# Performance work log

Hardware: AMD Instinct MI355X
Metric: run time of the kernel (lower is better)

Reference implementation:

```python
import jax, jax.numpy as jnp
import numpy as np

NP = 100000   # total patch-graph nodes
NG = 2000     # number of patch graphs == mesh nodes
EP = 800000   # patch edges
NM = 2000     # mesh nodes
EM = 32000    # mesh edges
FIN = 5       # patch_feat_dim
EPS = 1e-5


def _leaky(x, s):
    return jnp.where(x >= 0, x, s * x)


def _gat(x, W, al, ar, src, dst, n):
    # DGL GATConv (no bias/residual, eval mode): per-head projection,
    # additive attention with LeakyReLU(0.2), segment softmax over incoming
    # edges per destination, weighted scatter-sum.
    H, D = al.shape
    h = (x @ W).reshape(n, H, D)                  # [N,H,D]
    el = (h * al).sum(-1)                         # [N,H]
    er = (h * ar).sum(-1)                         # [N,H]
    e = _leaky(el[src] + er[dst], 0.2)            # [E,H]
    m = jax.ops.segment_max(e, dst, num_segments=n)
    ee = jnp.exp(e - m[dst])
    s = jax.ops.segment_sum(ee, dst, num_segments=n)
    a = ee / jnp.maximum(s, 1e-9)[dst]            # [E,H]
    return jax.ops.segment_sum(h[src] * a[:, :, None], dst, num_segments=n)


def _gnorm(x, g, b, al):
    # GraphNorm over all nodes in the batch (called without graph in source)
    mu = x.mean(0, keepdims=True)
    xc = x - al * mu
    v = (xc * xc).mean(0, keepdims=True)
    return g * xc / jnp.sqrt(v + EPS) + b


def setup_inputs() -> dict:
    key = jax.random.key(0)
    ks = jax.random.split(key, 40)
    w = lambda k, sh: jax.random.normal(k, sh, jnp.float32) * 0.1
    d = {}
    d['node_feats'] = jax.random.normal(ks[0], (NP, FIN), jnp.float32)
    d['patch_src'] = jax.random.randint(ks[1], (EP,), 0, NP)
    d['patch_dst'] = jax.random.randint(ks[2], (EP,), 0, NP)
    d['patch_gid'] = jnp.repeat(jnp.arange(NG), NP // NG)  # 50 nodes/graph
    d['mesh_src'] = jax.random.randint(ks[3], (EM,), 0, NM)
    d['mesh_dst'] = jax.random.randint(ks[4], (EM,), 0, NM)
    # PatchReader2GATLayer (hidden=64): GAT1 4h x64, GAT2 3h x64, GATcls 2h x32
    d['pW1'] = w(ks[5], (FIN, 256)); d['pal1'] = w(ks[6], (4, 64)); d['par1'] = w(ks[7], (4, 64))
    d['pg1_g'] = jnp.ones((256,)); d['pg1_b'] = jnp.zeros((256,)); d['pg1_a'] = jnp.ones((256,))
    d['pW2'] = w(ks[8], (256, 192)); d['pal2'] = w(ks[9], (3, 64)); d['par2'] = w(ks[10], (3, 64))
    d['pg2_g'] = jnp.ones((192,)); d['pg2_b'] = jnp.zeros((192,)); d['pg2_a'] = jnp.ones((192,))
    d['pW3'] = w(ks[11], (192, 64)); d['pal3'] = w(ks[12], (2, 32)); d['par3'] = w(ks[13], (2, 32))
    d['pcls'] = w(ks[14], (32, 32))
    # GraphNormPatchReader (readout_dim=32)
    d['rn_g'] = jnp.ones((32,)); d['rn_b'] = jnp.zeros((32,)); d['rn_a'] = jnp.ones((32,))
    # GraphMeshReader2GATLayer (hidden=64): GAT1 4h x64, GAT2 3h x32, GATcls 2h x32
    d['mW1'] = w(ks[15], (32, 256)); d['mal1'] = w(ks[16], (4, 64)); d['mar1'] = w(ks[17], (4, 64))
    d['mg1_g'] = jnp.ones((256,)); d['mg1_b'] = jnp.zeros((256,)); d['mg1_a'] = jnp.ones((256,))
    d['mW2'] = w(ks[18], (256, 96)); d['mal2'] = w(ks[19], (3, 32)); d['mar2'] = w(ks[20], (3, 32))
    d['mg2_g'] = jnp.ones((96,)); d['mg2_b'] = jnp.zeros((96,)); d['mg2_a'] = jnp.ones((96,))
    d['mW3'] = w(ks[21], (96, 64)); d['mal3'] = w(ks[22], (2, 32)); d['mar3'] = w(ks[23], (2, 32))
    d['mcls'] = w(ks[24], (32, 15))
    return d


def reference(node_feats, patch_src, patch_dst, patch_gid, mesh_src, mesh_dst,
              pW1, pal1, par1, pg1_g, pg1_b, pg1_a,
              pW2, pal2, par2, pg2_g, pg2_b, pg2_a,
              pW3, pal3, par3, pcls, rn_g, rn_b, rn_a,
              mW1, mal1, mar1, mg1_g, mg1_b, mg1_a,
              mW2, mal2, mar2, mg2_g, mg2_b, mg2_a,
              mW3, mal3, mar3, mcls):
    # ---- PatchReader2GATLayer over all batched patch graphs ----
    h = _gat(node_feats, pW1, pal1, par1, patch_src, patch_dst, NP).reshape(NP, -1)
    h = _gnorm(_leaky(h, 0.01), pg1_g, pg1_b, pg1_a)
    h = _gat(h, pW2, pal2, par2, patch_src, patch_dst, NP).reshape(NP, -1)
    h = _gnorm(_leaky(h, 0.01), pg2_g, pg2_b, pg2_a)
    h = _gat(h, pW3, pal3, par3, patch_src, patch_dst, NP).mean(1)  # [NP,32]
    cnt = jax.ops.segment_sum(jnp.ones((NP,), h.dtype), patch_gid, num_segments=NG)
    ro = jax.ops.segment_sum(h, patch_gid, num_segments=NG) / jnp.maximum(cnt, 1.0)[:, None]
    ro = ro @ pcls                                 # [NG,32] per-patch readouts
    ro = _gnorm(_leaky(ro, 0.01), rn_g, rn_b, rn_a)
    # ---- GraphMeshReader2GATLayer over mesh graph ----
    m = _gat(ro, mW1, mal1, mar1, mesh_src, mesh_dst, NM).reshape(NM, -1)
    m = _gnorm(_leaky(m, 0.01), mg1_g, mg1_b, mg1_a)
    m = _gat(m, mW2, mal2, mar2, mesh_src, mesh_dst, NM).reshape(NM, -1)
    m = _gnorm(_leaky(m, 0.01), mg2_g, mg2_b, mg2_a)
    m = _gat(m, mW3, mal3, mar3, mesh_src, mesh_dst, NM).mean(1)    # [NM,32]
    mesh_out = m.mean(0, keepdims=True) @ mcls     # dgl.mean_nodes -> [1,15]
    return (mesh_out, ro)
```

## Files before the change

### kernel.cpp

```cpp
#include <hip/hip_runtime.h>

typedef unsigned short ushort;
typedef unsigned int uint;
typedef __attribute__((ext_vector_type(8))) short short8;
typedef __attribute__((ext_vector_type(4))) float float4v;

#define DEV __device__ __forceinline__

DEV float b2f(ushort u) {
    union { uint i; float f; } v; v.i = ((uint)u) << 16; return v.f;
}
DEV ushort f2b(float f) {
    union { float f; uint i; } v; v.f = f;
    uint x = v.i;
    uint r = x + 0x7fffu + ((x >> 16) & 1u);
    return (ushort)(r >> 16);
}
DEV float leaky(float x, float s) { return x >= 0.f ? x : s * x; }

DEV void gload16(const void* g, void* l) {
    __builtin_amdgcn_global_load_lds((const __attribute__((address_space(1))) void*)g,
                                     (__attribute__((address_space(3))) void*)l, 16, 0, 0);
}

struct ConvArgs {
    const void* s[37];
    float* d[37];
    int n[37];
};

__global__ __launch_bounds__(256) void convert_kernel(ConvArgs a, const ushort* __restrict__ x0,
                                                      int* __restrict__ flag) {
    __shared__ int sfp32;
    int tid = threadIdx.x;
    if (tid < 64) {
        int cnt = 0;
        for (int j = 0; j < 8; j++) {
            ushort u = x0[(tid * 8 + j) * 2];
            int e = (u >> 7) & 0xFF;
            if (e >= 100 && e <= 140) cnt++;
        }
#pragma unroll
        for (int m = 1; m < 64; m <<= 1) cnt += __shfl_xor(cnt, m, 64);
        if (tid == 0) sfp32 = (cnt < 256) ? 1 : 0;
    }
    __syncthreads();
    bool fp32 = (sfp32 != 0);
    if (blockIdx.x == 0 && blockIdx.y == 0 && tid == 0) *flag = fp32 ? 1 : 0;

    int ai = blockIdx.y;
    int n = a.n[ai];
    const void* s = a.s[ai];
    float* d = a.d[ai];
    int stride = gridDim.x * blockDim.x;
    if (s == nullptr) {
        for (int i = blockIdx.x * blockDim.x + tid; i < n; i += stride) d[i] = 0.f;
    } else {
        for (int i = blockIdx.x * blockDim.x + tid; i < n; i += stride)
            d[i] = fp32 ? ((const float*)s)[i] : b2f(((const ushort*)s)[i]);
    }
}

struct PackArgs { const float* W; ushort* O; int K; int N; };
struct Pack5 { PackArgs m[5]; };

__global__ __launch_bounds__(256) void pack5_kernel(Pack5 pa) {
    int mi = blockIdx.y;
    const float* __restrict__ W = pa.m[mi].W;
    ushort* __restrict__ O = pa.m[mi].O;
    int K = pa.m[mi].K, N = pa.m[mi].N;
    int G = (K >> 3) * N;
    for (int gi = blockIdx.x * 256 + threadIdx.x; gi < G; gi += gridDim.x * 256) {
        int kb = gi / N;
        int n = gi - kb * N;
        const float* wp = W + (size_t)(kb * 8) * N + n;
        uint4 pk;
        pk.x = (uint)f2b(wp[0]) | ((uint)f2b(wp[N]) << 16);
        pk.y = (uint)f2b(wp[2 * N]) | ((uint)f2b(wp[3 * N]) << 16);
        pk.z = (uint)f2b(wp[4 * N]) | ((uint)f2b(wp[5 * N]) << 16);
        pk.w = (uint)f2b(wp[6 * N]) | ((uint)f2b(wp[7 * N]) << 16);
        *(uint4*)(O + (size_t)gi * 8) = pk;
    }
}

__global__ __launch_bounds__(256) void hist_both(const int* __restrict__ dstP, int* __restrict__ cntP, int EPc,
                                                 const int* __restrict__ dstM, int* __restrict__ cntM, int EMc,
                                                 int PB) {
    bool patch = (int)blockIdx.x < PB;
    const int* dst = patch ? dstP : dstM;
    int* cnt = patch ? cntP : cntM;
    int E = patch ? EPc : EMc;
    int nb = patch ? PB : gridDim.x - PB;
    int b = patch ? blockIdx.x : blockIdx.x - PB;
    int stride = nb * blockDim.x;
    for (int i = b * blockDim.x + threadIdx.x; i < E; i += stride)
        atomicAdd(&cnt[dst[i]], 1);
}

__global__ __launch_bounds__(256) void scan_both(const int* __restrict__ cntP, int* __restrict__ offP,
                                                 int* __restrict__ bsumP, int nP, int SBP,
                                                 const int* __restrict__ cntM, int* __restrict__ offM,
                                                 int* __restrict__ bsumM, int nM) {
    __shared__ int ls[256];
    bool patch = (int)blockIdx.x < SBP;
    const int* cnt = patch ? cntP : cntM;
    int* off = patch ? offP : offM;
    int* bsum = patch ? bsumP : bsumM;
    int n = patch ? nP : nM;
    int b = patch ? blockIdx.x : blockIdx.x - SBP;
    int t = threadIdx.x;
    int base = b * 2048 + t * 8;
    int v[8];
    int s = 0;
#pragma unroll
    for (int i = 0; i < 8; i++) {
        int idx = base + i;
        v[i] = idx < n ? cnt[idx] : 0;
        s += v[i];
    }
    ls[t] = s;
    __syncthreads();
#pragma unroll
    for (int d = 1; d < 256; d <<= 1) {
        int add = (t >= d) ? ls[t - d] : 0;
        __syncthreads();
        ls[t] += add;
        __syncthreads();
    }
    int run = ls[t] - s;
#pragma unroll
    for (int i = 0; i < 8; i++) {
        int idx = base + i;
        if (idx < n) off[idx] = run;
        run += v[i];
    }
    if (t == 255) bsum[b] = ls[255];
}

__global__ __launch_bounds__(256) void fixup_both(const int* __restrict__ bsumP, int* __restrict__ offP,
                                                  int nP, int SBP,
                                                  const int* __restrict__ bsumM, int* __restrict__ offM,
                                                  int nM, int SBM) {
    bool patch = (int)blockIdx.x < SBP;
    const int* bsum = patch ? bsumP : bsumM;
    int* off = patch ? offP : offM;
    int n = patch ? nP : nM;
    int nb = patch ? SBP : SBM;
    int b = patch ? blockIdx.x : blockIdx.x - SBP;
    int t = threadIdx.x;
    int base = 0;
    for (int i = 0; i < b; i++) base += bsum[i];
    int idx0 = b * 2048 + t * 8;
    if (base != 0) {
#pragma unroll
        for (int i = 0; i < 8; i++) {
            int idx = idx0 + i;
            if (idx < n) off[idx] += base;
        }
    }
    if (b == nb - 1 && t == 255) off[n] = base + bsum[b];
}

__global__ __launch_bounds__(256) void scatter_both(const int* __restrict__ srcP, const int* __restrict__ dstP,
                                                    const int* __restrict__ offP, int* __restrict__ curP,
                                                    int* __restrict__ csrP, int EPc,
                                                    const int* __restrict__ srcM, const int* __restrict__ dstM,
                                                    const int* __restrict__ offM, int* __restrict__ curM,
                                                    int* __restrict__ csrM, int EMc, int PB) {
    bool patch = (int)blockIdx.x < PB;
    const int* src = patch ? srcP : srcM;
    const int* dst = patch ? dstP : dstM;
    const int* off = patch ? offP : offM;
    int* cursor = patch ? curP : curM;
    int* csr = patch ? csrP : csrM;
    int E = patch ? EPc : EMc;
    int nb = patch ? PB : gridDim.x - PB;
    int b = patch ? blockIdx.x : blockIdx.x - PB;
    int stride = nb * blockDim.x;
    for (int i = b * blockDim.x + threadIdx.x; i < E; i += stride) {
        int d = dst[i];
        int pos = off[d] + atomicAdd(&cursor[d], 1);
        csr[pos] = src[i];
    }
}

__global__ __launch_bounds__(256) void proj1_elr_kernel(const float* __restrict__ x,
                                                        const float* __restrict__ W,
                                                        const float* __restrict__ al,
                                                        const float* __restrict__ ar,
                                                        float* __restrict__ el,
                                                        float* __restrict__ er, int Nn) {
    int t = threadIdx.x;
    int head = t >> 6, lane = t & 63;
    float wv[5];
#pragma unroll
    for (int k = 0; k < 5; k++) wv[k] = W[k * 256 + t];
    float alv = al[t];
    float arv = ar[t];
    int n0 = blockIdx.x * 4;
    int n1 = min(n0 + 4, Nn);
    for (int n = n0; n < n1; n++) {
        float acc = 0.f;
#pragma unroll
        for (int k = 0; k < 5; k++) acc += x[n * 5 + k] * wv[k];
        float pl = acc * alv, pr = acc * arv;
#pragma unroll
        for (int m = 1; m < 64; m <<= 1) {
            pl += __shfl_xor(pl, m, 64);
            pr += __shfl_xor(pr, m, 64);
        }
        if (lane == 0) { el[n * 4 + head] = pl; er[n * 4 + head] = pr; }
    }
}

__global__ __launch_bounds__(256, 4) void aggr1_fly_kernel(const float* __restrict__ x,
                                                           const float* __restrict__ W,
                                                           const float* __restrict__ el,
                                                           const float* __restrict__ er,
                                                           const int* __restrict__ off,
                                                           const int* __restrict__ csr,
                                                           float* __restrict__ out, int Nn) {
    int wid = threadIdx.x >> 6;
    int lane = threadIdx.x & 63;
    int grp = lane / 20;
    int gl = lane - grp * 20;
    int dbase = blockIdx.x * 12 + wid * 3;
    int d = dbase + grp;
    bool accl = (grp < 3) && (d < Nn);
    int dd = accl ? d : 0;
    int h_ = gl / 5, k_ = gl - h_ * 5;
    int c0 = lane * 4;
    int myhead = lane >> 4;
    float w0[5], w1[5], w2[5], w3[5];
#pragma unroll
    for (int k = 0; k < 5; k++) {
        float4 wv = *(const float4*)(W + k * 256 + c0);
        w0[k] = wv.x; w1[k] = wv.y; w2[k] = wv.z; w3[k] = wv.w;
    }
    float erd = accl ? er[dd * 4 + h_] : 0.f;
    float acc = 0.f, sh = 0.f;
    int e = accl ? off[dd] : 0;
    int e1 = accl ? off[dd + 1] : 0;
#define A1_ACC(XV, EV)                                  \
    {                                                   \
        float e0_ = (EV) + erd;                         \
        e0_ = e0_ >= 0.f ? e0_ : 0.2f * e0_;            \
        float w_ = __expf(fminf(e0_, 80.f));            \
        acc += w_ * (XV);                               \
        sh += w_;                                       \
    }
    for (; e + 4 <= e1; e += 4) {
        int s0 = csr[e], s1 = csr[e + 1], s2 = csr[e + 2], s3 = csr[e + 3];
        float x0 = x[s0 * 5 + k_];
        float x1 = x[s1 * 5 + k_];
        float x2 = x[s2 * 5 + k_];
        float x3 = x[s3 * 5 + k_];
        float v0 = el[s0 * 4 + h_];
        float v1 = el[s1 * 4 + h_];
        float v2 = el[s2 * 4 + h_];
        float v3 = el[s3 * 4 + h_];
        A1_ACC(x0, v0) A1_ACC(x1, v1) A1_ACC(x2, v2) A1_ACC(x3, v3)
    }
    for (; e < e1; e++) {
        int s0 = csr[e];
        float x0 = x[s0 * 5 + k_];
        float v0 = el[s0 * 4 + h_];
        A1_ACC(x0, v0)
    }
#undef A1_ACC
#pragma unroll
    for (int g3 = 0; g3 < 3; g3++) {
        int dsto = dbase + g3;
        if (dsto >= Nn) break;
        float a_k[5];
#pragma unroll
        for (int k = 0; k < 5; k++) a_k[k] = __shfl(acc, g3 * 20 + myhead * 5 + k, 64);
        float s = __shfl(sh, g3 * 20 + myhead * 5, 64);
        float inv = 1.f / fmaxf(s, 1e-9f);
        float o0 = 0.f, o1 = 0.f, o2 = 0.f, o3 = 0.f;
#pragma unroll
        for (int k = 0; k < 5; k++) {
            o0 += a_k[k] * w0[k]; o1 += a_k[k] * w1[k];
            o2 += a_k[k] * w2[k]; o3 += a_k[k] * w3[k];
        }
        float4 o;
        o.x = leaky(o0 * inv, 0.01f);
        o.y = leaky(o1 * inv, 0.01f);
        o.z = leaky(o2 * inv, 0.01f);
        o.w = leaky(o3 * inv, 0.01f);
        *(float4*)(out + (size_t)dsto * 256 + c0) = o;
    }
}

template <int H, int LOGD, int HD>
__global__ __launch_bounds__(256, 4) void aggr4_kernel(const ushort* __restrict__ h,
                                                       const float* __restrict__ el,
                                                       const float* __restrict__ er,
                                                       const int* __restrict__ off,
                                                       const int* __restrict__ csr,
                                                       float* __restrict__ out, int Nn,
                                                       float oslope) {
    int wid = threadIdx.x >> 6;
    int lane = threadIdx.x & 63;
    int half = lane >> 5, hl = lane & 31;
    constexpr int NL = HD / 8;
    int d = blockIdx.x * 8 + wid * 2 + half;
    bool valid = (hl < NL) && (d < Nn);
    int dd = valid ? d : 0;
    int myhead = (hl * 8) >> LOGD;
    float erd = valid ? er[dd * H + myhead] : 0.f;
    float a0 = 0.f, a1 = 0.f, a2 = 0.f, a3 = 0.f;
    float a4 = 0.f, a5 = 0.f, a6 = 0.f, a7 = 0.f, s = 0.f;
    int e = valid ? off[dd] : 0;
    int e1 = valid ? off[dd + 1] : 0;
#define A8_ACC(EV, HR)                                      \
    {                                                       \
        float ev_ = (EV) + erd;                             \
        ev_ = ev_ >= 0.f ? ev_ : 0.2f * ev_;                \
        float w_ = __expf(fminf(ev_, 80.f));                \
        a0 += w_ * b2f((ushort)(HR).x);                     \
        a1 += w_ * b2f((ushort)((HR).x >> 16));             \
        a2 += w_ * b2f((ushort)(HR).y);                     \
        a3 += w_ * b2f((ushort)((HR).y >> 16));             \
        a4 += w_ * b2f((ushort)(HR).z);                     \
        a5 += w_ * b2f((ushort)((HR).z >> 16));             \
        a6 += w_ * b2f((ushort)(HR).w);                     \
        a7 += w_ * b2f((ushort)((HR).w >> 16));             \
        s += w_;                                            \
    }
#define A8_ACCM(OK, EV, HR)                                 \
    {                                                       \
        float ev_ = (EV) + erd;                             \
        ev_ = ev_ >= 0.f ? ev_ : 0.2f * ev_;                \
        float w_ = (OK) ? __expf(fminf(ev_, 80.f)) : 0.f;   \
        a0 += w_ * b2f((ushort)(HR).x);                     \
        a1 += w_ * b2f((ushort)((HR).x >> 16));             \
        a2 += w_ * b2f((ushort)(HR).y);                     \
        a3 += w_ * b2f((ushort)((HR).y >> 16));             \
        a4 += w_ * b2f((ushort)(HR).z);                     \
        a5 += w_ * b2f((ushort)((HR).z >> 16));             \
        a6 += w_ * b2f((ushort)(HR).w);                     \
        a7 += w_ * b2f((ushort)((HR).w >> 16));             \
        s += w_;                                            \
    }
    for (; e + 4 <= e1; e += 4) {
        int s0 = csr[e], s1 = csr[e + 1], s2 = csr[e + 2], s3 = csr[e + 3];
        float e0 = el[s0 * H + myhead];
        float e1v = el[s1 * H + myhead];
        float e2v = el[s2 * H + myhead];
        float e3v = el[s3 * H + myhead];
        uint4 h0 = *(const uint4*)(h + (size_t)s0 * HD + hl * 8);
        uint4 h1 = *(const uint4*)(h + (size_t)s1 * HD + hl * 8);
        uint4 h2 = *(const uint4*)(h + (size_t)s2 * HD + hl * 8);
        uint4 h3 = *(const uint4*)(h + (size_t)s3 * HD + hl * 8);
        A8_ACC(e0, h0) A8_ACC(e1v, h1) A8_ACC(e2v, h2) A8_ACC(e3v, h3)
    }
    if (e < e1) {
        bool k1 = e + 1 < e1, k2 = e + 2 < e1, k3 = e + 3 < e1;
        int s0 = csr[e];
        int s1 = csr[k1 ? e + 1 : e];
        int s2 = csr[k2 ? e + 2 : e];
        int s3 = csr[k3 ? e + 3 : e];
        float e0 = el[s0 * H + myhead];
        float e1v = el[s1 * H + myhead];
        float e2v = el[s2 * H + myhead];
        float e3v = el[s3 * H + myhead];
        uint4 h0 = *(const uint4*)(h + (size_t)s0 * HD + hl * 8);
        uint4 h1 = *(const uint4*)(h + (size_t)s1 * HD + hl * 8);
        uint4 h2 = *(const uint4*)(h + (size_t)s2 * HD + hl * 8);
        uint4 h3 = *(const uint4*)(h + (size_t)s3 * HD + hl * 8);
        A8_ACCM(true, e0, h0) A8_ACCM(k1, e1v, h1) A8_ACCM(k2, e2v, h2) A8_ACCM(k3, e3v, h3)
    }
#undef A8_ACC
#undef A8_ACCM
    if (valid) {
        float inv = 1.f / fmaxf(s, 1e-9f);
        float4 oa, ob;
        oa.x = leaky(a0 * inv, oslope);
        oa.y = leaky(a1 * inv, oslope);
        oa.z = leaky(a2 * inv, oslope);
        oa.w = leaky(a3 * inv, oslope);
        ob.x = leaky(a4 * inv, oslope);
        ob.y = leaky(a5 * inv, oslope);
        ob.z = leaky(a6 * inv, oslope);
        ob.w = leaky(a7 * inv, oslope);
        float* po = out + (size_t)dd * HD + hl * 8;
        *(float4*)(po) = oa;
        *(float4*)(po + 4) = ob;
    }
}

__global__ __launch_bounds__(256, 4) void aggr_mean_kernel(const ushort* __restrict__ h,
                                                           const float* __restrict__ el,
                                                           const float* __restrict__ er,
                                                           const int* __restrict__ off,
                                                           const int* __restrict__ csr,
                                                           const int* __restrict__ gid,
                                                           float* __restrict__ out_sum,
                                                           float* __restrict__ out_cnt,
                                                           int Nn) {
    __shared__ float red[8][32];
    __shared__ int gids[8];
    int wid = threadIdx.x >> 6;
    int lane = threadIdx.x & 63;
    int half = lane >> 5;
    int hl = lane & 31;
    int row = wid * 2 + half;
    int d = blockIdx.x * 8 + row;
    bool valid = d < Nn;
    int dd = valid ? d : 0;
    int head = hl >> 4;
    float erd = er[dd * 2 + head];
    float a0 = 0.f, a1 = 0.f, s = 0.f;
    int e = valid ? off[dd] : 0;
    int e1 = valid ? off[dd + 1] : 0;
#define AM_ACC(Q, V)                                        \
    {                                                       \
        float ev_ = (head ? (Q).y : (Q).x) + erd;           \
        ev_ = ev_ >= 0.f ? ev_ : 0.2f * ev_;                \
        float w_ = __expf(fminf(ev_, 80.f));                \
        a0 += w_ * b2f((ushort)(V));                        \
        a1 += w_ * b2f((ushort)((V) >> 16));                \
        s += w_;                                            \
    }
#define AM_ACCM(OK, Q, V)                                   \
    {                                                       \
        float ev_ = (head ? (Q).y : (Q).x) + erd;           \
        ev_ = ev_ >= 0.f ? ev_ : 0.2f * ev_;                \
        float w_ = (OK) ? __expf(fminf(ev_, 80.f)) : 0.f;   \
        a0 += w_ * b2f((ushort)(V));                        \
        a1 += w_ * b2f((ushort)((V) >> 16));                \
        s += w_;                                            \
    }
    for (; e + 8 <= e1; e += 8) {
        int s0 = csr[e], s1 = csr[e + 1], s2 = csr[e + 2], s3 = csr[e + 3];
        int s4 = csr[e + 4], s5 = csr[e + 5], s6 = csr[e + 6], s7 = csr[e + 7];
        float2 q0 = *(const float2*)(el + s0 * 2);
        float2 q1 = *(const float2*)(el + s1 * 2);
        float2 q2 = *(const float2*)(el + s2 * 2);
        float2 q3 = *(const float2*)(el + s3 * 2);
        float2 q4 = *(const float2*)(el + s4 * 2);
        float2 q5 = *(const float2*)(el + s5 * 2);
        float2 q6 = *(const float2*)(el + s6 * 2);
        float2 q7 = *(const float2*)(el + s7 * 2);
        uint v0 = *(const uint*)(h + (size_t)s0 * 64 + hl * 2);
        uint v1 = *(const uint*)(h + (size_t)s1 * 64 + hl * 2);
        uint v2 = *(const uint*)(h + (size_t)s2 * 64 + hl * 2);
        uint v3 = *(const uint*)(h + (size_t)s3 * 64 + hl * 2);
        uint v4 = *(const uint*)(h + (size_t)s4 * 64 + hl * 2);
        uint v5 = *(const uint*)(h + (size_t)s5 * 64 + hl * 2);
        uint v6 = *(const uint*)(h + (size_t)s6 * 64 + hl * 2);
        uint v7 = *(const uint*)(h + (size_t)s7 * 64 + hl * 2);
        AM_ACC(q0, v0) AM_ACC(q1, v1) AM_ACC(q2, v2) AM_ACC(q3, v3)
        AM_ACC(q4, v4) AM_ACC(q5, v5) AM_ACC(q6, v6) AM_ACC(q7, v7)
    }
    if (e < e1) {
        bool k1 = e + 1 < e1, k2 = e + 2 < e1, k3 = e + 3 < e1;
        bool k4 = e + 4 < e1, k5 = e + 5 < e1, k6 = e + 6 < e1, k7 = e + 7 < e1;
        int s0 = csr[e];
        int s1 = csr[k1 ? e + 1 : e];
        int s2 = csr[k2 ? e + 2 : e];
        int s3 = csr[k3 ? e + 3 : e];
        int s4 = csr[k4 ? e + 4 : e];
        int s5 = csr[k5 ? e + 5 : e];
        int s6 = csr[k6 ? e + 6 : e];
        int s7 = csr[k7 ? e + 7 : e];
        float2 q0 = *(const float2*)(el + s0 * 2);
        float2 q1 = *(const float2*)(el + s1 * 2);
        float2 q2 = *(const float2*)(el + s2 * 2);
        float2 q3 = *(const float2*)(el + s3 * 2);
        float2 q4 = *(const float2*)(el + s4 * 2);
        float2 q5 = *(const float2*)(el + s5 * 2);
        float2 q6 = *(const float2*)(el + s6 * 2);
        float2 q7 = *(const float2*)(el + s7 * 2);
        uint v0 = *(const uint*)(h + (size_t)s0 * 64 + hl * 2);
        uint v1 = *(const uint*)(h + (size_t)s1 * 64 + hl * 2);
        uint v2 = *(const uint*)(h + (size_t)s2 * 64 + hl * 2);
        uint v3 = *(const uint*)(h + (size_t)s3 * 64 + hl * 2);
        uint v4 = *(const uint*)(h + (size_t)s4 * 64 + hl * 2);
        uint v5 = *(const uint*)(h + (size_t)s5 * 64 + hl * 2);
        uint v6 = *(const uint*)(h + (size_t)s6 * 64 + hl * 2);
        uint v7 = *(const uint*)(h + (size_t)s7 * 64 + hl * 2);
        AM_ACCM(true, q0, v0) AM_ACCM(k1, q1, v1) AM_ACCM(k2, q2, v2) AM_ACCM(k3, q3, v3)
        AM_ACCM(k4, q4, v4) AM_ACCM(k5, q5, v5) AM_ACCM(k6, q6, v6) AM_ACCM(k7, q7, v7)
    }
#undef AM_ACC
#undef AM_ACCM
    float inv = 1.f / fmaxf(s, 1e-9f);
    float y0 = a0 * inv, y1 = a1 * inv;
    float p0 = __shfl(y0, lane + 16, 64);
    float p1 = __shfl(y1, lane + 16, 64);
    if (hl < 16) {
        red[row][2 * hl] = valid ? 0.5f * (y0 + p0) : 0.f;
        red[row][2 * hl + 1] = valid ? 0.5f * (y1 + p1) : 0.f;
        if (hl == 0) gids[row] = valid ? (gid ? gid[d] : 0) : -1;
    }
    __syncthreads();
    if (threadIdx.x < 32) {
        int c = threadIdx.x;
        float sum = 0.f;
        int cur = gids[0];
#pragma unroll
        for (int r = 0; r < 8; r++) {
            int gr = gids[r];
            if (gr != cur) {
                if (cur >= 0) atomicAdd(&out_sum[cur * 32 + c], sum);
                sum = 0.f;
                cur = gr;
            }
            if (gr >= 0) sum += red[r][c];
        }
        if (cur >= 0) atomicAdd(&out_sum[cur * 32 + c], sum);
    } else if (threadIdx.x == 32 && out_cnt) {
        float cnt = 0.f;
        int cur = gids[0];
#pragma unroll
        for (int r = 0; r < 8; r++) {
            int gr = gids[r];
            if (gr != cur) {
                if (cur >= 0) atomicAdd(&out_cnt[cur], cnt);
                cnt = 0.f;
                cur = gr;
            }
            if (gr >= 0) cnt += 1.f;
        }
        if (cur >= 0) atomicAdd(&out_cnt[cur], cnt);
    }
}

__global__ void colstats_kernel(const float* __restrict__ x,
                                float* __restrict__ sum,
                                float* __restrict__ sumsq, int Nn) {
    int C = blockDim.x, c = threadIdx.x;
    int nb = gridDim.x;
    int chunk = (Nn + nb - 1) / nb;
    int r0 = blockIdx.x * chunk;
    int r1 = min(r0 + chunk, Nn);
    float ls = 0.f, lq = 0.f;
    int r = r0;
    for (; r + 8 <= r1; r += 8) {
        const float* p = x + (size_t)r * C + c;
        float v0 = p[0];
        float v1 = p[C];
        float v2 = p[2 * C];
        float v3 = p[3 * C];
        float v4 = p[4 * C];
        float v5 = p[5 * C];
        float v6 = p[6 * C];
        float v7 = p[7 * C];
        ls += ((v0 + v1) + (v2 + v3)) + ((v4 + v5) + (v6 + v7));
        lq += ((v0 * v0 + v1 * v1) + (v2 * v2 + v3 * v3)) +
              ((v4 * v4 + v5 * v5) + (v6 * v6 + v7 * v7));
    }
    for (; r < r1; r++) {
        float v = x[(size_t)r * C + c];
        ls += v; lq += v * v;
    }
    atomicAdd(&sum[c], ls);
    atomicAdd(&sumsq[c], lq);
}

__global__ void gnorm_apply_ro_kernel(const float* __restrict__ x,
                                      const float* __restrict__ sum,
                                      const float* __restrict__ sumsq,
                                      const float* __restrict__ g,
                                      const float* __restrict__ b,
                                      const float* __restrict__ a,
                                      void* __restrict__ doutv,
                                      const int* __restrict__ flag,
                                      float* __restrict__ rof, int Nn) {
    int c = threadIdx.x;
    float invn = 1.f / (float)Nn;
    float mu = sum[c] * invn, ex2 = sumsq[c] * invn;
    float av = a[c];
    float var = ex2 - 2.f * av * mu * mu + av * av * mu * mu;
    float sc = g[c] * rsqrtf(var + 1e-5f);
    float sh = b[c] - sc * av * mu;
    bool fp32 = (*flag != 0);
    for (int r = blockIdx.x; r < Nn; r += gridDim.x) {
        int i = r * 32 + c;
        float v = x[i] * sc + sh;
        rof[i] = v;
        if (fp32) ((float*)doutv)[15 + i] = v;
        else      ((ushort*)doutv)[15 + i] = f2b(v);
    }
}

__global__ __launch_bounds__(256) void readout_kernel(const float* __restrict__ ro_sum,
                                                      const float* __restrict__ ro_cnt,
                                                      const float* __restrict__ pcls,
                                                      float* __restrict__ ro_lin, int NGc) {
    int idx = blockIdx.x * blockDim.x + threadIdx.x;
    int g = idx >> 5, c = idx & 31;
    if (g >= NGc) return;
    float inv = 1.f / fmaxf(ro_cnt[g], 1.f);
    float acc = 0.f;
#pragma unroll
    for (int k = 0; k < 32; k++) acc += ro_sum[g * 32 + k] * inv * pcls[k * 32 + c];
    ro_lin[g * 32 + c] = leaky(acc, 0.01f);
}

template <int K, int N, int H, int LOGD, bool GN>
__global__ __launch_bounds__(256, 4) void gemm_bf_kernel(const float* __restrict__ A,
                                                         const ushort* __restrict__ Bc,
                                                         const float* __restrict__ csum,
                                                         const float* __restrict__ g,
                                                         const float* __restrict__ gb,
                                                         const float* __restrict__ ga,
                                                         const float* __restrict__ al,
                                                         const float* __restrict__ ar,
                                                         ushort* __restrict__ C,
                                                         float* __restrict__ el,
                                                         float* __restrict__ er, int M) {
    constexpr int NT = N / 16;
    constexpr int T = K / 32;
    constexpr int BG = 4 * N;
    constexpr int RB = (BG + 255) / 256;
    __shared__ __align__(16) ushort Blds[2][BG * 8];
    __shared__ float ScL[K], ShL[K];
    int tid = threadIdx.x;
    int w = tid >> 6, lane = tid & 63, q = lane >> 4, l16 = lane & 15;
    int m0 = blockIdx.x * 64;
    if constexpr (GN) {
        if (tid < K) {
            float invn = 1.f / (float)M;
            float mu = csum[tid] * invn, ex2 = csum[512 + tid] * invn;
            float av = ga[tid];
            float var = ex2 - 2.f * av * mu * mu + av * av * mu * mu;
            float sc = g[tid] * rsqrtf(var + 1e-5f);
            ScL[tid] = sc;
            ShL[tid] = gb[tid] - sc * av * mu;
        }
    }
    int row = m0 + w * 16 + l16;
    const float* ap = A + (size_t)(row < M ? row : 0) * K + q * 8;

#pragma unroll
    for (int rb = 0; rb < RB; rb++) {
        int gidx = rb * 256 + tid;
        if (BG % 256 == 0 || gidx < BG) gload16(Bc + (size_t)gidx * 8, &Blds[0][gidx * 8]);
    }
    float4 a0 = *(const float4*)(ap);
    float4 a1 = *(const float4*)(ap + 4);
    float4v acc[NT];
#pragma unroll
    for (int nt = 0; nt < NT; nt++) acc[nt] = (float4v){0.f, 0.f, 0.f, 0.f};
    __syncthreads();

    int cur = 0;
    for (int t = 0; t < T; t++) {
        float4 n0, n1;
        bool more = (t + 1 < T);
        if (more) {
#pragma unroll
            for (int rb = 0; rb < RB; rb++) {
                int gidx = rb * 256 + tid;
                if (BG % 256 == 0 || gidx < BG)
                    gload16(Bc + (size_t)((t + 1) * BG + gidx) * 8, &Blds[cur ^ 1][gidx * 8]);
            }
            n0 = *(const float4*)(ap + (t + 1) * 32);
            n1 = *(const float4*)(ap + (t + 1) * 32 + 4);
        }
        if constexpr (GN) {
            int kc = t * 32 + q * 8;
            float4 sc0 = *(const float4*)(&ScL[kc]);
            float4 sc1 = *(const float4*)(&ScL[kc + 4]);
            float4 sh0 = *(const float4*)(&ShL[kc]);
            float4 sh1 = *(const float4*)(&ShL[kc + 4]);
            a0.x = a0.x * sc0.x + sh0.x;
            a0.y = a0.y * sc0.y + sh0.y;
            a0.z = a0.z * sc0.z + sh0.z;
            a0.w = a0.w * sc0.w + sh0.w;
            a1.x = a1.x * sc1.x + sh1.x;
            a1.y = a1.y * sc1.y + sh1.y;
            a1.z = a1.z * sc1.z + sh1.z;
            a1.w = a1.w * sc1.w + sh1.w;
        }
        union { uint4 u; short8 s; } cvt;
        cvt.u.x = (uint)f2b(a0.x) | ((uint)f2b(a0.y) << 16);
        cvt.u.y = (uint)f2b(a0.z) | ((uint)f2b(a0.w) << 16);
        cvt.u.z = (uint)f2b(a1.x) | ((uint)f2b(a1.y) << 16);
        cvt.u.w = (uint)f2b(a1.z) | ((uint)f2b(a1.w) << 16);
        short8 av = cvt.s;
#pragma unroll
        for (int nt = 0; nt < NT; nt++) {
            short8 bv = *(const short8*)(&Blds[cur][(q * N + nt * 16 + l16) * 8]);
            acc[nt] = __builtin_amdgcn_mfma_f32_16x16x32_bf16(av, bv, acc[nt], 0, 0, 0);
        }
        __syncthreads();
        if (more) { a0 = n0; a1 = n1; }
        cur ^= 1;
    }
    float pel[4][H], per[4][H];
#pragma unroll
    for (int i = 0; i < 4; i++)
#pragma unroll
        for (int hh = 0; hh < H; hh++) { pel[i][hh] = 0.f; per[i][hh] = 0.f; }
#pragma unroll
    for (int nt = 0; nt < NT; nt++) {
        int col = nt * 16 + l16;
        float alc = al[col], arc = ar[col];
        constexpr int HSH = LOGD - 4;
        int hh = nt >> HSH;
#pragma unroll
        for (int i = 0; i < 4; i++) {
            int orow = m0 + w * 16 + q * 4 + i;
            float v = acc[nt][i];
            if (orow < M) C[(size_t)orow * N + col] = f2b(v);
            pel[i][hh] += v * alc;
            per[i][hh] += v * arc;
        }
    }
#pragma unroll
    for (int i = 0; i < 4; i++) {
#pragma unroll
        for (int hh = 0; hh < H; hh++) {
            float vl = pel[i][hh], vr = per[i][hh];
#pragma unroll
            for (int m = 1; m < 16; m <<= 1) {
                vl += __shfl_xor(vl, m, 64);
                vr += __shfl_xor(vr, m, 64);
            }
            if (l16 == 0) {
                int orow = m0 + w * 16 + q * 4 + i;
                if (orow < M) { el[orow * H + hh] = vl; er[orow * H + hh] = vr; }
            }
        }
    }
}

__global__ __launch_bounds__(64) void final_kernel(const float* __restrict__ msum,
                                                   const float* __restrict__ mcls,
                                                   void* __restrict__ doutv,
                                                   const int* __restrict__ flag, int Nm) {
    int t = threadIdx.x;
    if (t < 15) {
        float inv = 1.f / (float)Nm;
        float acc = 0.f;
#pragma unroll
        for (int c = 0; c < 32; c++) acc += msum[c] * inv * mcls[c * 15 + t];
        if (*flag) ((float*)doutv)[t] = acc;
        else       ((ushort*)doutv)[t] = f2b(acc);
    }
}

extern "C" void kernel_launch(void* const* d_in, const int* in_sizes, int n_in,
                              void* d_out, int out_size, void* d_ws, size_t ws_size,
                              hipStream_t stream) {
    const int NP = 100000, NG = 2000, EP = 800000, NM = 2000, EM = 32000;

    const int* patch_src = (const int*)d_in[1];
    const int* patch_dst = (const int*)d_in[2];
    const int* patch_gid = (const int*)d_in[3];
    const int* mesh_src = (const int*)d_in[4];
    const int* mesh_dst = (const int*)d_in[5];

    char* p = (char*)d_ws;
    auto alloc = [&](size_t bytes) -> char* {
        char* r = p;
        p += (bytes + 255) & ~(size_t)255;
        return r;
    };
    char* zbase = p;
    int* cnt_p = (int*)alloc((size_t)NP * 4);
    int* cursor_p = (int*)alloc((size_t)NP * 4);
    int* cnt_m = (int*)alloc((size_t)NM * 4);
    int* cursor_m = (int*)alloc((size_t)NM * 4);
    float* ro_sum = (float*)alloc((size_t)NG * 32 * 4);
    float* ro_cnt = (float*)alloc((size_t)NG * 4);
    float* msum = (float*)alloc(32 * 4);
    float* colbuf = (float*)alloc(6 * 1024 * 4);
    size_t zbytes = (size_t)(p - zbase);
    int* flag = (int*)alloc(256);
    int* off_p = (int*)alloc((size_t)(NP + 1) * 4);
    int* off_m = (int*)alloc((size_t)(NM + 1) * 4);
    int* bsum_p = (int*)alloc(64 * 4);
    int* bsum_m = (int*)alloc(16 * 4);
    int* csr_p = (int*)alloc((size_t)EP * 4);
    int* csr_m = (int*)alloc((size_t)EM * 4);
    float* el = (float*)alloc((size_t)NP * 4 * 4);
    float* er = (float*)alloc((size_t)NP * 4 * 4);
    ushort* hbuf = (ushort*)alloc((size_t)NP * 256 * 2);
    float* gbuf = (float*)alloc((size_t)NP * 256 * 4);
    ushort* hm = (ushort*)alloc((size_t)NM * 256 * 2);
    float* gm = (float*)alloc((size_t)NM * 256 * 4);
    float* elm = (float*)alloc((size_t)NM * 4 * 4);
    float* erm = (float*)alloc((size_t)NM * 4 * 4);
    float* ro_lin = (float*)alloc((size_t)NG * 32 * 4);
    float* ro_f = (float*)alloc((size_t)NG * 32 * 4);
    ushort* Bp2 = (ushort*)alloc(256 * 192 * 2);
    ushort* Bp3 = (ushort*)alloc(192 * 64 * 2);
    ushort* Bm1 = (ushort*)alloc(32 * 256 * 2);
    ushort* Bm2 = (ushort*)alloc(256 * 96 * 2);
    ushort* Bm3 = (ushort*)alloc(96 * 64 * 2);

    ConvArgs ca;
    float* convp[36];
    int conv_idx[36];
    conv_idx[0] = 0;
    for (int i = 1; i < 36; i++) conv_idx[i] = 5 + i;
    for (int j = 0; j < 36; j++) {
        int ii = conv_idx[j];
        int n = in_sizes[ii];
        float* dd = (float*)alloc((size_t)n * 4);
        ca.s[j] = d_in[ii];
        ca.d[j] = dd;
        ca.n[j] = n;
        convp[j] = dd;
    }
    ca.s[36] = nullptr;
    ca.d[36] = (float*)zbase;
    ca.n[36] = (int)(zbytes / 4);

    const float* xf = convp[0];
    const float *pW1f = convp[1], *pal1f = convp[2], *par1f = convp[3];
    const float *pg1_gf = convp[4], *pg1_bf = convp[5], *pg1_af = convp[6];
    const float *pW2f = convp[7], *pal2f = convp[8], *par2f = convp[9];
    const float *pg2_gf = convp[10], *pg2_bf = convp[11], *pg2_af = convp[12];
    const float *pW3f = convp[13], *pal3f = convp[14], *par3f = convp[15];
    const float* pclsf = convp[16];
    const float *rn_gf = convp[17], *rn_bf2 = convp[18], *rn_af = convp[19];
    const float *mW1f = convp[20], *mal1f = convp[21], *mar1f = convp[22];
    const float *mg1_gf = convp[23], *mg1_bf = convp[24], *mg1_af = convp[25];
    const float *mW2f = convp[26], *mal2f = convp[27], *mar2f = convp[28];
    const float *mg2_gf = convp[29], *mg2_bf = convp[30], *mg2_af = convp[31];
    const float *mW3f = convp[32], *mal3f = convp[33], *mar3f = convp[34];
    const float* mclsf = convp[35];

    convert_kernel<<<dim3(16, 37), 256, 0, stream>>>(ca, (const ushort*)d_in[0], flag);

    Pack5 p5;
    p5.m[0] = {pW2f, Bp2, 256, 192};
    p5.m[1] = {pW3f, Bp3, 192, 64};
    p5.m[2] = {mW1f, Bm1, 32, 256};
    p5.m[3] = {mW2f, Bm2, 256, 96};
    p5.m[4] = {mW3f, Bm3, 96, 64};
    pack5_kernel<<<dim3(48, 5), 256, 0, stream>>>(p5);

    const int SBP = (NP + 2047) / 2048, SBM = (NM + 2047) / 2048;
    hist_both<<<512 + 64, 256, 0, stream>>>(patch_dst, cnt_p, EP, mesh_dst, cnt_m, EM, 512);
    scan_both<<<SBP + SBM, 256, 0, stream>>>(cnt_p, off_p, bsum_p, NP, SBP, cnt_m, off_m, bsum_m, NM);
    fixup_both<<<SBP + SBM, 256, 0, stream>>>(bsum_p, off_p, NP, SBP, bsum_m, off_m, NM, SBM);
    scatter_both<<<512 + 64, 256, 0, stream>>>(patch_src, patch_dst, off_p, cursor_p, csr_p, EP,
                                               mesh_src, mesh_dst, off_m, cursor_m, csr_m, EM, 512);

    int gP = (NP + 3) / 4;
    int gP12 = (NP + 11) / 12;
    int gA2 = (NP + 7) / 8, gA2m = (NM + 7) / 8;
    int gP2 = (NP + 7) / 8, gM2 = (NM + 7) / 8;
    int gT = (NP + 63) / 64, gTm = (NM + 63) / 64;
    float* cb0 = colbuf + 0 * 1024;
    float* cb1 = colbuf + 1 * 1024;
    float* cb2 = colbuf + 2 * 1024;
    float* cb3 = colbuf + 3 * 1024;
    float* cb4 = colbuf + 4 * 1024;

    proj1_elr_kernel<<<gP, 256, 0, stream>>>(xf, pW1f, pal1f, par1f, el, er, NP);
    aggr1_fly_kernel<<<gP12, 256, 0, stream>>>(xf, pW1f, el, er, off_p, csr_p, gbuf, NP);
    colstats_kernel<<<512, 256, 0, stream>>>(gbuf, cb0, cb0 + 512, NP);

    gemm_bf_kernel<256, 192, 3, 6, true><<<gT, 256, 0, stream>>>(
        gbuf, Bp2, cb0, pg1_gf, pg1_bf, pg1_af, pal2f, par2f, hbuf, el, er, NP);
    aggr4_kernel<3, 6, 192><<<gA2, 256, 0, stream>>>(hbuf, el, er, off_p, csr_p, gbuf, NP, 0.01f);
    colstats_kernel<<<512, 192, 0, stream>>>(gbuf, cb1, cb1 + 512, NP);

    gemm_bf_kernel<192, 64, 2, 5, true><<<gT, 256, 0, stream>>>(
        gbuf, Bp3, cb1, pg2_gf, pg2_bf, pg2_af, pal3f, par3f, hbuf, el, er, NP);
    aggr_mean_kernel<<<gP2, 256, 0, stream>>>(hbuf, el, er, off_p, csr_p, patch_gid,
                                              ro_sum, ro_cnt, NP);

    readout_kernel<<<(NG * 32 + 255) / 256, 256, 0, stream>>>(ro_sum, ro_cnt, pclsf, ro_lin, NG);
    colstats_kernel<<<64, 32, 0, stream>>>(ro_lin, cb2, cb2 + 512, NG);
    gnorm_apply_ro_kernel<<<64, 32, 0, stream>>>(ro_lin, cb2, cb2 + 512, rn_gf, rn_bf2, rn_af,
                                                 d_out, flag, ro_f, NG);

    gemm_bf_kernel<32, 256, 4, 6, false><<<gTm, 256, 0, stream>>>(
        ro_f, Bm1, nullptr, nullptr, nullptr, nullptr, mal1f, mar1f, hm, elm, erm, NM);
    aggr4_kernel<4, 6, 256><<<gA2m, 256, 0, stream>>>(hm, elm, erm, off_m, csr_m, gm, NM, 0.01f);
    colstats_kernel<<<64, 256, 0, stream>>>(gm, cb3, cb3 + 512, NM);

    gemm_bf_kernel<256, 96, 3, 5, true><<<gTm, 256, 0, stream>>>(
        gm, Bm2, cb3, mg1_gf, mg1_bf, mg1_af, mal2f, mar2f, hm, elm, erm, NM);
    aggr4_kernel<3, 5, 96><<<gA2m, 256, 0, stream>>>(hm, elm, erm, off_m, csr_m, gm, NM, 0.01f);
    colstats_kernel<<<64, 96, 0, stream>>>(gm, cb4, cb4 + 512, NM);

    gemm_bf_kernel<96, 64, 2, 5, true><<<gTm, 256, 0, stream>>>(
        gm, Bm3, cb4, mg2_gf, mg2_bf, mg2_af, mal3f, mar3f, hm, elm, erm, NM);
    aggr_mean_kernel<<<gM2, 256, 0, stream>>>(hm, elm, erm, off_m, csr_m, nullptr,
                                              msum, nullptr, NM);
    final_kernel<<<1, 64, 0, stream>>>(msum, mclsf, d_out, flag, NM);

    (void)n_in; (void)out_size; (void)ws_size;
}
```

Baseline: 645.3 us.

## Fuse GraphNorm column statistics into aggregation kernels and precompute W·a for layer-1 attention

```diff
diff --git a/kernel.cpp b/kernel.cpp
--- a/kernel.cpp
+++ b/kernel.cpp
@@ -80,6 +80,25 @@
         pk.z = (uint)f2b(wp[4 * N]) | ((uint)f2b(wp[5 * N]) << 16);
         pk.w = (uint)f2b(wp[6 * N]) | ((uint)f2b(wp[7 * N]) << 16);
         *(uint4*)(O + (size_t)gi * 8) = pk;
+    }
+}
+
+__global__ __launch_bounds__(64) void prep_elr_kernel(const float* __restrict__ W,
+                                                      const float* __restrict__ al,
+                                                      const float* __restrict__ ar,
+                                                      float* __restrict__ wal,
+                                                      float* __restrict__ war) {
+    int t = threadIdx.x;
+    if (t < 20) {
+        int k = t >> 2, h = t & 3;
+        float sl = 0.f, sr = 0.f;
+        for (int d = 0; d < 64; d++) {
+            float w = W[k * 256 + h * 64 + d];
+            sl += w * al[h * 64 + d];
+            sr += w * ar[h * 64 + d];
+        }
+        wal[t] = sl;
+        war[t] = sr;
     }
 }
 
@@ -184,33 +203,32 @@
     }
 }
 
-__global__ __launch_bounds__(256) void proj1_elr_kernel(const float* __restrict__ x,
-                                                        const float* __restrict__ W,
-                                                        const float* __restrict__ al,
-                                                        const float* __restrict__ ar,
-                                                        float* __restrict__ el,
-                                                        float* __restrict__ er, int Nn) {
-    int t = threadIdx.x;
-    int head = t >> 6, lane = t & 63;
-    float wv[5];
-#pragma unroll
-    for (int k = 0; k < 5; k++) wv[k] = W[k * 256 + t];
-    float alv = al[t];
-    float arv = ar[t];
-    int n0 = blockIdx.x * 4;
-    int n1 = min(n0 + 4, Nn);
-    for (int n = n0; n < n1; n++) {
-        float acc = 0.f;
-#pragma unroll
-        for (int k = 0; k < 5; k++) acc += x[n * 5 + k] * wv[k];
-        float pl = acc * alv, pr = acc * arv;
-#pragma unroll
-        for (int m = 1; m < 64; m <<= 1) {
-            pl += __shfl_xor(pl, m, 64);
-            pr += __shfl_xor(pr, m, 64);
-        }
-        if (lane == 0) { el[n * 4 + head] = pl; er[n * 4 + head] = pr; }
-    }
+__global__ __launch_bounds__(256) void proj1b_kernel(const float* __restrict__ x,
+                                                     const float* __restrict__ wal,
+                                                     const float* __restrict__ war,
+                                                     float* __restrict__ el,
+                                                     float* __restrict__ er, int Nn) {
+    int n = blockIdx.x * 256 + threadIdx.x;
+    if (n >= Nn) return;
+    float xv[5];
+#pragma unroll
+    for (int k = 0; k < 5; k++) xv[k] = x[n * 5 + k];
+    float l0 = 0.f, l1 = 0.f, l2 = 0.f, l3 = 0.f;
+    float r0 = 0.f, r1 = 0.f, r2 = 0.f, r3 = 0.f;
+#pragma unroll
+    for (int k = 0; k < 5; k++) {
+        float xk = xv[k];
+        l0 += xk * wal[k * 4 + 0];
+        l1 += xk * wal[k * 4 + 1];
+        l2 += xk * wal[k * 4 + 2];
+        l3 += xk * wal[k * 4 + 3];
+        r0 += xk * war[k * 4 + 0];
+        r1 += xk * war[k * 4 + 1];
+        r2 += xk * war[k * 4 + 2];
+        r3 += xk * war[k * 4 + 3];
+    }
+    *(float4*)(el + n * 4) = make_float4(l0, l1, l2, l3);
+    *(float4*)(er + n * 4) = make_float4(r0, r1, r2, r3);
 }
 
 __global__ __launch_bounds__(256, 4) void aggr1_fly_kernel(const float* __restrict__ x,
@@ -219,7 +237,10 @@
                                                            const float* __restrict__ er,
                                                            const int* __restrict__ off,
                                                            const int* __restrict__ csr,
-                                                           float* __restrict__ out, int Nn) {
+                                                           float* __restrict__ out,
+                                                           float* __restrict__ cstat, int Nn) {
+    __shared__ float s1m[4][256];
+    __shared__ float s1q[4][256];
     int wid = threadIdx.x >> 6;
     int lane = threadIdx.x & 63;
     int grp = lane / 20;
@@ -268,6 +289,8 @@
         A1_ACC(x0, v0)
     }
 #undef A1_ACC
+    float ls0 = 0.f, ls1 = 0.f, ls2 = 0.f, ls3 = 0.f;
+    float lq0 = 0.f, lq1 = 0.f, lq2 = 0.f, lq3 = 0.f;
 #pragma unroll
     for (int g3 = 0; g3 < 3; g3++) {
         int dsto = dbase + g3;
@@ -289,7 +312,21 @@
         o.z = leaky(o2 * inv, 0.01f);
         o.w = leaky(o3 * inv, 0.01f);
         *(float4*)(out + (size_t)dsto * 256 + c0) = o;
-    }
+        ls0 += o.x; lq0 += o.x * o.x;
+        ls1 += o.y; lq1 += o.y * o.y;
+        ls2 += o.z; lq2 += o.z * o.z;
+        ls3 += o.w; lq3 += o.w * o.w;
+    }
+    *(float4*)&s1m[wid][c0] = make_float4(ls0, ls1, ls2, ls3);
+    *(float4*)&s1q[wid][c0] = make_float4(lq0, lq1, lq2, lq3);
+    __syncthreads();
+    int tid = threadIdx.x;
+    float ssv = 0.f, sqv = 0.f;
+#pragma unroll
+    for (int w8 = 0; w8 < 4; w8++) { ssv += s1m[w8][tid]; sqv += s1q[w8][tid]; }
+    float* dst = cstat + (size_t)(blockIdx.x & 7) * 1024;
+    atomicAdd(dst + tid, ssv);
+    atomicAdd(dst + 512 + tid, sqv);
 }
 
 template <int H, int LOGD, int HD>
@@ -298,8 +335,11 @@
                                                        const float* __restrict__ er,
                                                        const int* __restrict__ off,
                                                        const int* __restrict__ csr,
-                                                       float* __restrict__ out, int Nn,
+                                                       float* __restrict__ out,
+                                                       float* __restrict__ cstat, int Nn,
                                                        float oslope) {
+    __shared__ float ssm[8][HD];
+    __shared__ float ssq[8][HD];
     int wid = threadIdx.x >> 6;
     int lane = threadIdx.x & 63;
     int half = lane >> 5, hl = lane & 31;
@@ -373,20 +413,39 @@
     }
 #undef A8_ACC
 #undef A8_ACCM
+    float o0 = 0.f, o1 = 0.f, o2 = 0.f, o3 = 0.f;
+    float o4 = 0.f, o5 = 0.f, o6 = 0.f, o7 = 0.f;
     if (valid) {
         float inv = 1.f / fmaxf(s, 1e-9f);
-        float4 oa, ob;
-        oa.x = leaky(a0 * inv, oslope);
-        oa.y = leaky(a1 * inv, oslope);
-        oa.z = leaky(a2 * inv, oslope);
-        oa.w = leaky(a3 * inv, oslope);
-        ob.x = leaky(a4 * inv, oslope);
-        ob.y = leaky(a5 * inv, oslope);
-        ob.z = leaky(a6 * inv, oslope);
-        ob.w = leaky(a7 * inv, oslope);
+        o0 = leaky(a0 * inv, oslope);
+        o1 = leaky(a1 * inv, oslope);
+        o2 = leaky(a2 * inv, oslope);
+        o3 = leaky(a3 * inv, oslope);
+        o4 = leaky(a4 * inv, oslope);
+        o5 = leaky(a5 * inv, oslope);
+        o6 = leaky(a6 * inv, oslope);
+        o7 = leaky(a7 * inv, oslope);
         float* po = out + (size_t)dd * HD + hl * 8;
-        *(float4*)(po) = oa;
-        *(float4*)(po + 4) = ob;
+        *(float4*)(po) = make_float4(o0, o1, o2, o3);
+        *(float4*)(po + 4) = make_float4(o4, o5, o6, o7);
+    }
+    int r = wid * 2 + half;
+    if (hl < NL) {
+        int cb = hl * 8;
+        *(float4*)&ssm[r][cb] = make_float4(o0, o1, o2, o3);
+        *(float4*)&ssm[r][cb + 4] = make_float4(o4, o5, o6, o7);
+        *(float4*)&ssq[r][cb] = make_float4(o0 * o0, o1 * o1, o2 * o2, o3 * o3);
+        *(float4*)&ssq[r][cb + 4] = make_float4(o4 * o4, o5 * o5, o6 * o6, o7 * o7);
+    }
+    __syncthreads();
+    int tid = threadIdx.x;
+    if (tid < HD) {
+        float sv = 0.f, qv = 0.f;
+#pragma unroll
+        for (int rr = 0; rr < 8; rr++) { sv += ssm[rr][tid]; qv += ssq[rr][tid]; }
+        float* dst = cstat + (size_t)(blockIdx.x & 7) * 1024;
+        atomicAdd(dst + tid, sv);
+        atomicAdd(dst + 512 + tid, qv);
     }
 }
 
@@ -528,41 +587,8 @@
     }
 }
 
-__global__ void colstats_kernel(const float* __restrict__ x,
-                                float* __restrict__ sum,
-                                float* __restrict__ sumsq, int Nn) {
-    int C = blockDim.x, c = threadIdx.x;
-    int nb = gridDim.x;
-    int chunk = (Nn + nb - 1) / nb;
-    int r0 = blockIdx.x * chunk;
-    int r1 = min(r0 + chunk, Nn);
-    float ls = 0.f, lq = 0.f;
-    int r = r0;
-    for (; r + 8 <= r1; r += 8) {
-        const float* p = x + (size_t)r * C + c;
-        float v0 = p[0];
-        float v1 = p[C];
-        float v2 = p[2 * C];
-        float v3 = p[3 * C];
-        float v4 = p[4 * C];
-        float v5 = p[5 * C];
-        float v6 = p[6 * C];
-        float v7 = p[7 * C];
-        ls += ((v0 + v1) + (v2 + v3)) + ((v4 + v5) + (v6 + v7));
-        lq += ((v0 * v0 + v1 * v1) + (v2 * v2 + v3 * v3)) +
-              ((v4 * v4 + v5 * v5) + (v6 * v6 + v7 * v7));
-    }
-    for (; r < r1; r++) {
-        float v = x[(size_t)r * C + c];
-        ls += v; lq += v * v;
-    }
-    atomicAdd(&sum[c], ls);
-    atomicAdd(&sumsq[c], lq);
-}
-
 __global__ void gnorm_apply_ro_kernel(const float* __restrict__ x,
-                                      const float* __restrict__ sum,
-                                      const float* __restrict__ sumsq,
+                                      const float* __restrict__ cstat,
                                       const float* __restrict__ g,
                                       const float* __restrict__ b,
                                       const float* __restrict__ a,
@@ -570,8 +596,14 @@
                                       const int* __restrict__ flag,
                                       float* __restrict__ rof, int Nn) {
     int c = threadIdx.x;
+    float cs = 0.f, cq = 0.f;
+#pragma unroll
+    for (int s8 = 0; s8 < 8; s8++) {
+        cs += cstat[s8 * 1024 + c];
+        cq += cstat[s8 * 1024 + 512 + c];
+    }
     float invn = 1.f / (float)Nn;
-    float mu = sum[c] * invn, ex2 = sumsq[c] * invn;
+    float mu = cs * invn, ex2 = cq * invn;
     float av = a[c];
     float var = ex2 - 2.f * av * mu * mu + av * av * mu * mu;
     float sc = g[c] * rsqrtf(var + 1e-5f);
@@ -589,15 +621,31 @@
 __global__ __launch_bounds__(256) void readout_kernel(const float* __restrict__ ro_sum,
                                                       const float* __restrict__ ro_cnt,
                                                       const float* __restrict__ pcls,
-                                                      float* __restrict__ ro_lin, int NGc) {
-    int idx = blockIdx.x * blockDim.x + threadIdx.x;
+                                                      float* __restrict__ ro_lin,
+                                                      float* __restrict__ cstat, int NGc) {
+    __shared__ float ss[32], sq[32];
+    int tid = threadIdx.x;
+    if (tid < 32) { ss[tid] = 0.f; sq[tid] = 0.f; }
+    __syncthreads();
+    int idx = blockIdx.x * 256 + tid;
     int g = idx >> 5, c = idx & 31;
-    if (g >= NGc) return;
-    float inv = 1.f / fmaxf(ro_cnt[g], 1.f);
-    float acc = 0.f;
-#pragma unroll
-    for (int k = 0; k < 32; k++) acc += ro_sum[g * 32 + k] * inv * pcls[k * 32 + c];
-    ro_lin[g * 32 + c] = leaky(acc, 0.01f);
+    float v = 0.f;
+    if (g < NGc) {
+        float inv = 1.f / fmaxf(ro_cnt[g], 1.f);
+        float acc = 0.f;
+#pragma unroll
+        for (int k = 0; k < 32; k++) acc += ro_sum[g * 32 + k] * inv * pcls[k * 32 + c];
+        v = leaky(acc, 0.01f);
+        ro_lin[g * 32 + c] = v;
+    }
+    atomicAdd(&ss[c], v);
+    atomicAdd(&sq[c], v * v);
+    __syncthreads();
+    if (tid < 32) {
+        float* dst = cstat + (size_t)(blockIdx.x & 7) * 1024;
+        atomicAdd(dst + tid, ss[tid]);
+        atomicAdd(dst + 512 + tid, sq[tid]);
+    }
 }
 
 template <int K, int N, int H, int LOGD, bool GN>
@@ -623,8 +671,14 @@
     int m0 = blockIdx.x * 64;
     if constexpr (GN) {
         if (tid < K) {
+            float cs = 0.f, cq = 0.f;
+#pragma unroll
+            for (int s8 = 0; s8 < 8; s8++) {
+                cs += csum[s8 * 1024 + tid];
+                cq += csum[s8 * 1024 + 512 + tid];
+            }
             float invn = 1.f / (float)M;
-            float mu = csum[tid] * invn, ex2 = csum[512 + tid] * invn;
+            float mu = cs * invn, ex2 = cq * invn;
             float av = ga[tid];
             float var = ex2 - 2.f * av * mu * mu + av * av * mu * mu;
             float sc = g[tid] * rsqrtf(var + 1e-5f);
@@ -769,7 +823,7 @@
     float* ro_sum = (float*)alloc((size_t)NG * 32 * 4);
     float* ro_cnt = (float*)alloc((size_t)NG * 4);
     float* msum = (float*)alloc(32 * 4);
-    float* colbuf = (float*)alloc(6 * 1024 * 4);
+    float* colbuf = (float*)alloc((size_t)5 * 8 * 1024 * 4);
     size_t zbytes = (size_t)(p - zbase);
     int* flag = (int*)alloc(256);
     int* off_p = (int*)alloc((size_t)(NP + 1) * 4);
@@ -793,6 +847,8 @@
     ushort* Bm1 = (ushort*)alloc(32 * 256 * 2);
     ushort* Bm2 = (ushort*)alloc(256 * 96 * 2);
     ushort* Bm3 = (ushort*)alloc(96 * 64 * 2);
+    float* wal1 = (float*)alloc(20 * 4);
+    float* war1 = (float*)alloc(20 * 4);
 
     ConvArgs ca;
     float* convp[36];
@@ -836,6 +892,7 @@
     p5.m[3] = {mW2f, Bm2, 256, 96};
     p5.m[4] = {mW3f, Bm3, 96, 64};
     pack5_kernel<<<dim3(48, 5), 256, 0, stream>>>(p5);
+    prep_elr_kernel<<<1, 64, 0, stream>>>(pW1f, pal1f, par1f, wal1, war1);
 
     const int SBP = (NP + 2047) / 2048, SBM = (NM + 2047) / 2048;
     hist_both<<<512 + 64, 256, 0, stream>>>(patch_dst, cnt_p, EP, mesh_dst, cnt_m, EM, 512);
@@ -844,45 +901,39 @@
     scatter_both<<<512 + 64, 256, 0, stream>>>(patch_src, patch_dst, off_p, cursor_p, csr_p, EP,
                                                mesh_src, mesh_dst, off_m, cursor_m, csr_m, EM, 512);
 
-    int gP = (NP + 3) / 4;
     int gP12 = (NP + 11) / 12;
     int gA2 = (NP + 7) / 8, gA2m = (NM + 7) / 8;
     int gP2 = (NP + 7) / 8, gM2 = (NM + 7) / 8;
     int gT = (NP + 63) / 64, gTm = (NM + 63) / 64;
-    float* cb0 = colbuf + 0 * 1024;
-    float* cb1 = colbuf + 1 * 1024;
-    float* cb2 = colbuf + 2 * 1024;
-    float* cb3 = colbuf + 3 * 1024;
-    float* cb4 = colbuf + 4 * 1024;
-
-    proj1_elr_kernel<<<gP, 256, 0, stream>>>(xf, pW1f, pal1f, par1f, el, er, NP);
-    aggr1_fly_kernel<<<gP12, 256, 0, stream>>>(xf, pW1f, el, er, off_p, csr_p, gbuf, NP);
-    colstats_kernel<<<512, 256, 0, stream>>>(gbuf, cb0, cb0 + 512, NP);
+    float* cb0 = colbuf + 0 * 8192;
+    float* cb1 = colbuf + 1 * 8192;
+    float* cb2 = colbuf + 2 * 8192;
+    float* cb3 = colbuf + 3 * 8192;
+    float* cb4 = colbuf + 4 * 8192;
+
+    proj1b_kernel<<<(NP + 255) / 256, 256, 0, stream>>>(xf, wal1, war1, el, er, NP);
+    aggr1_fly_kernel<<<gP12, 256, 0, stream>>>(xf, pW1f, el, er, off_p, csr_p, gbuf, cb0, NP);
 
     gemm_bf_kernel<256, 192, 3, 6, true><<<gT, 256, 0, stream>>>(
         gbuf, Bp2, cb0, pg1_gf, pg1_bf, pg1_af, pal2f, par2f, hbuf, el, er, NP);
-    aggr4_kernel<3, 6, 192><<<gA2, 256, 0, stream>>>(hbuf, el, er, off_p, csr_p, gbuf, NP, 0.01f);
-    colstats_kernel<<<512, 192, 0, stream>>>(gbuf, cb1, cb1 + 512, NP);
+    aggr4_kernel<3, 6, 192><<<gA2, 256, 0, stream>>>(hbuf, el, er, off_p, csr_p, gbuf, cb1, NP, 0.01f);
 
     gemm_bf_kernel<192, 64, 2, 5, true><<<gT, 256, 0, stream>>>(
         gbuf, Bp3, cb1, pg2_gf, pg2_bf, pg2_af, pal3f, par3f, hbuf, el, er, NP);
     aggr_mean_kernel<<<gP2, 256, 0, stream>>>(hbuf, el, er, off_p, csr_p, patch_gid,
                                               ro_sum, ro_cnt, NP);
 
-    readout_kernel<<<(NG * 32 + 255) / 256, 256, 0, stream>>>(ro_sum, ro_cnt, pclsf, ro_lin, NG);
-    colstats_kernel<<<64, 32, 0, stream>>>(ro_lin, cb2, cb2 + 512, NG);
-    gnorm_apply_ro_kernel<<<64, 32, 0, stream>>>(ro_lin, cb2, cb2 + 512, rn_gf, rn_bf2, rn_af,
+    readout_kernel<<<(NG * 32 + 255) / 256, 256, 0, stream>>>(ro_sum, ro_cnt, pclsf, ro_lin, cb2, NG);
+    gnorm_apply_ro_kernel<<<64, 32, 0, stream>>>(ro_lin, cb2, rn_gf, rn_bf2, rn_af,
                                                  d_out, flag, ro_f, NG);
 
     gemm_bf_kernel<32, 256, 4, 6, false><<<gTm, 256, 0, stream>>>(
         ro_f, Bm1, nullptr, nullptr, nullptr, nullptr, mal1f, mar1f, hm, elm, erm, NM);
-    aggr4_kernel<4, 6, 256><<<gA2m, 256, 0, stream>>>(hm, elm, erm, off_m, csr_m, gm, NM, 0.01f);
-    colstats_kernel<<<64, 256, 0, stream>>>(gm, cb3, cb3 + 512, NM);
+    aggr4_kernel<4, 6, 256><<<gA2m, 256, 0, stream>>>(hm, elm, erm, off_m, csr_m, gm, cb3, NM, 0.01f);
 
     gemm_bf_kernel<256, 96, 3, 5, true><<<gTm, 256, 0, stream>>>(
         gm, Bm2, cb3, mg1_gf, mg1_bf, mg1_af, mal2f, mar2f, hm, elm, erm, NM);
-    aggr4_kernel<3, 5, 96><<<gA2m, 256, 0, stream>>>(hm, elm, erm, off_m, csr_m, gm, NM, 0.01f);
-    colstats_kernel<<<64, 96, 0, stream>>>(gm, cb4, cb4 + 512, NM);
+    aggr4_kernel<3, 5, 96><<<gA2m, 256, 0, stream>>>(hm, elm, erm, off_m, csr_m, gm, cb4, NM, 0.01f);
 
     gemm_bf_kernel<96, 64, 2, 5, true><<<gTm, 256, 0, stream>>>(
         gm, Bm3, cb4, mg2_gf, mg2_bf, mg2_af, mal3f, mar3f, hm, elm, erm, NM);
```

New measurement: 559.5 us. -13.3%, faster.
